# Kernel optimization log

Measured on AMD Instinct MI355X. Metric: run time of the kernel, lower is better.

Reference implementation:

```python
import jax, jax.numpy as jnp
import numpy as np
from jax import lax

N, L, V, ES, HS = 16384, 512, 32000, 32, 64


def setup_inputs() -> dict:
    key = jax.random.key(0)
    k_tok, k_len, k_emb, k_wih, k_whh, k_bih, k_bhh = jax.random.split(key, 7)
    # valid tokens in [1, V) so that (x != 0).sum(1) == true prefix length
    tok = jax.random.randint(k_tok, (N, L), 1, V)
    lengths = jax.random.randint(k_len, (N,), 0, L + 1)  # includes empty seqs
    x = jnp.where(jnp.arange(L)[None, :] < lengths[:, None], tok, 0)
    s = 0.1
    embedding = jax.random.normal(k_emb, (V, ES), dtype=jnp.float32) * s
    w_ih = jax.random.normal(k_wih, (3 * HS, ES), dtype=jnp.float32) * s  # [r|z|n] stacked (torch order)
    w_hh = jax.random.normal(k_whh, (3 * HS, HS), dtype=jnp.float32) * s
    b_ih = jax.random.normal(k_bih, (3 * HS,), dtype=jnp.float32) * s
    b_hh = jax.random.normal(k_bhh, (3 * HS,), dtype=jnp.float32) * s
    return {"x": x, "embedding": embedding, "w_ih": w_ih, "w_hh": w_hh,
            "b_ih": b_ih, "b_hh": b_hh}


def reference(x, embedding, w_ih, w_hh, b_ih, b_hh):
    # Faithful math: final GRU hidden state over the nonzero prefix of each row;
    # rows with length 0 return zeros (h0). Equivalent to bucketed
    # pack_padded_sequence + GRU + scatter of final hidden states.
    n, l = x.shape
    hs = w_hh.shape[1]
    lengths = (x != 0).sum(axis=1)  # [n]

    def step(h, inp):
        t, xt = inp                      # xt: [n] token ids at time t
        e = embedding[xt]                # [n, es] gather
        gx = e @ w_ih.T + b_ih           # [n, 3*hs]
        gh = h @ w_hh.T + b_hh           # [n, 3*hs]
        xr, xz, xn = jnp.split(gx, 3, axis=-1)
        hr, hz, hn = jnp.split(gh, 3, axis=-1)
        r = jax.nn.sigmoid(xr + hr)
        z = jax.nn.sigmoid(xz + hz)
        ng = jnp.tanh(xn + r * hn)
        h_new = (1.0 - z) * ng + z * h   # torch GRU update
        h = jnp.where((t < lengths)[:, None], h_new, h)  # freeze past length
        return h, None

    h0 = jnp.zeros((n, hs), dtype=embedding.dtype)
    hT, _ = lax.scan(step, h0, (jnp.arange(l), x.T))
    return hT
```

## Files before the change

kernel.cpp:

```cpp
#include <hip/hip_runtime.h>

#define N_SEQ 16384
#define LSEQ  512
#define VOCAB 32000
#define ES    32
#define HS    64
#define LDH   72

#define SC_RZ (-1.4426950408889634f)
#define SC_N  (-2.8853900817779268f)

typedef _Float16 v8h __attribute__((ext_vector_type(8)));
typedef float    v4f __attribute__((ext_vector_type(4)));

#define NLB (N_SEQ / 4)
#define NEB (VOCAB * ES / 256)
__global__ __launch_bounds__(256) void k_prep(const int* __restrict__ x,
                                              const float* __restrict__ emb,
                                              const float* __restrict__ whh,
                                              const float* __restrict__ wih,
                                              int* __restrict__ len,
                                              int* __restrict__ hist,
                                              _Float16* __restrict__ ef,
                                              _Float16* __restrict__ wpk,
                                              _Float16* __restrict__ wpe){
  int b = blockIdx.x;
  if (b < NLB){
    int wid  = (b * 256 + threadIdx.x) >> 6;
    int lane = threadIdx.x & 63;
    const int* xr = x + (size_t)wid * LSEQ;
    int cnt = 0;
    #pragma unroll
    for (int j = 0; j < 8; ++j) cnt += (xr[lane + 64*j] != 0) ? 1 : 0;
    #pragma unroll
    for (int o = 32; o; o >>= 1) cnt += __shfl_down(cnt, o, 64);
    if (lane == 0){ len[wid] = cnt; atomicAdd(&hist[cnt], 1); }
  } else if (b < NLB + NEB){
    int i = (b - NLB) * 256 + threadIdx.x;
    ef[i] = (_Float16)emb[i];
  } else if (b < NLB + NEB + 6){
    int tid = (b - NLB - NEB) * 256 + threadIdx.x;
    int f = tid >> 6, l = tid & 63;
    int jt = f >> 1, kf = f & 1;
    float sc = (jt < 8) ? SC_RZ : SC_N;
    #pragma unroll
    for (int i = 0; i < 8; ++i){
      int row = jt * 16 + (l & 15);
      int col = kf * 32 + (l >> 4) * 8 + i;
      wpk[(size_t)tid * 8 + i] = (_Float16)(sc * whh[row * HS + col]);
    }
  } else {
    int tid = (b - NLB - NEB - 6) * 256 + threadIdx.x;
    int tile = tid >> 6, l = tid & 63;
    float sc = ((tile >> 2) < 2) ? SC_RZ : SC_N;
    #pragma unroll
    for (int i = 0; i < 8; ++i){
      int row = tile * 16 + (l & 15);
      int col = (l >> 4) * 8 + i;
      wpe[(size_t)tid * 8 + i] = (_Float16)(sc * wih[row * ES + col]);
    }
  }
}

__global__ __launch_bounds__(1024) void k_sort(const int* __restrict__ hist,
                                               const int* __restrict__ len,
                                               int* __restrict__ perm){
  __shared__ int buf[1024];
  __shared__ int offs[513];
  int i = threadIdx.x;
  buf[i] = (i < 513) ? hist[i] : 0;
  __syncthreads();
  for (int d = 1; d < 1024; d <<= 1){
    int v = (i >= d) ? buf[i - d] : 0;
    __syncthreads();
    buf[i] += v;
    __syncthreads();
  }
  if (i < 513) offs[i] = (i == 0) ? 0 : buf[i - 1];
  __syncthreads();
  for (int s = i; s < N_SEQ; s += 1024){
    int l = len[s];
    int pos = atomicAdd(&offs[l], 1);
    perm[pos] = s;
  }
}

__global__ __launch_bounds__(256, 4) void k_gru(
    const int* __restrict__ x, const _Float16* __restrict__ ef,
    const _Float16* __restrict__ wpk, const _Float16* __restrict__ wpe,
    const float* __restrict__ bih, const float* __restrict__ bhh,
    const int* __restrict__ perm, const int* __restrict__ len,
    float* __restrict__ out)
{
  __shared__ __align__(16) _Float16 hb[2][16 * LDH];
  int qt   = threadIdx.x >> 6;
  int w = blockIdx.x >> 8, cq = blockIdx.x & 255;
  int rank = w * 256 + ((w & 1) ? (255 - cq) : cq);
  int grp  = 1023 - rank;
  int lane = threadIdx.x & 63;
  int q = lane >> 4, c = lane & 15;
  int uu = qt*16 + c;

  v8h bfh[3][2], bfe[3];
  #pragma unroll
  for (int g = 0; g < 3; ++g){
    int tile = g*4 + qt;
    #pragma unroll
    for (int kf = 0; kf < 2; ++kf)
      bfh[g][kf] = *(const v8h*)(wpk + ((size_t)(tile*2 + kf)*64 + lane)*8);
    bfe[g] = *(const v8h*)(wpe + ((size_t)tile*64 + lane)*8);
  }

  int sq[4], ln[4];
  #pragma unroll
  for (int r = 0; r < 4; ++r){
    int s = perm[grp * 16 + q*4 + r];
    sq[r] = s;
    ln[r] = len[s];
  }
  float br  = SC_RZ * (bih[uu]      + bhh[uu]);
  float bz  = SC_RZ * (bih[HS + uu] + bhh[HS + uu]);
  float ben = SC_N  *  bih[2*HS + uu];
  float bhn = SC_N  *  bhh[2*HS + uu];
  v4f brq  = {br, br, br, br};
  v4f bzq  = {bz, bz, bz, bz};
  v4f benq = {ben, ben, ben, ben};
  v4f bhnq = {bhn, bhn, bhn, bhn};

  float h[4];
  #pragma unroll
  for (int r = 0; r < 4; ++r) h[r] = 0.f;

  for (int i = threadIdx.x; i < 16*LDH; i += 256) hb[0][i] = (_Float16)0.f;
  __syncthreads();

  int tmax = max(max(ln[0], ln[1]), max(ln[2], ln[3]));
  tmax = max(tmax, __shfl_xor(tmax, 16, 64));
  tmax = max(tmax, __shfl_xor(tmax, 32, 64));
  int tmin = min(min(ln[0], ln[1]), min(ln[2], ln[3]));
  tmin = min(tmin, __shfl_xor(tmin, 16, 64));
  tmin = min(tmin, __shfl_xor(tmin, 32, 64));

  const int* xr = x + (size_t)perm[grp * 16 + c] * LSEQ;

  v8h aec, aen;
  int tk1, tk2;
  v4f pra, prb, pza, pzb, dea, deb;
  {
    int tk0 = xr[0];
    aec = *(const v8h*)(ef + (size_t)tk0 * ES + q*8);
    tk1 = xr[1];
    pra = __builtin_amdgcn_mfma_f32_16x16x32_f16(aec, bfe[0], brq,  0,0,0);
    pza = __builtin_amdgcn_mfma_f32_16x16x32_f16(aec, bfe[1], bzq,  0,0,0);
    dea = __builtin_amdgcn_mfma_f32_16x16x32_f16(aec, bfe[2], benq, 0,0,0);
  }

  #define LDS_BARRIER() __asm__ volatile("s_waitcnt lgkmcnt(0)\n\ts_barrier" ::: "memory")

  #define GRU_STEP(FREEZE, AEN, PRR, PRZ, DEN, PRRn, PRZn, DENn, TKN_, TKNN_, RB, WB) \
  {                                                                            \
    AEN = *(const v8h*)(ef + (size_t)TKN_ * ES + q*8);       \
    int t2 = min(t + 2, LSEQ - 1);                                             \
    TKNN_ = xr[t2];                                             \
    v8h a0 = *(const v8h*)(&hb[RB][c*LDH + q*8]);                              \
    v8h a1 = *(const v8h*)(&hb[RB][c*LDH + 32 + q*8]);                         \
    v4f zr  = __builtin_amdgcn_mfma_f32_16x16x32_f16(a1, bfh[0][1], PRR, 0,0,0);\
    v4f Dr  = __builtin_amdgcn_mfma_f32_16x16x32_f16(a0, bfh[0][0], zr,  0,0,0);\
    v4f zz  = __builtin_amdgcn_mfma_f32_16x16x32_f16(a1, bfh[1][1], PRZ, 0,0,0);\
    v4f Dz  = __builtin_amdgcn_mfma_f32_16x16x32_f16(a0, bfh[1][0], zz,  0,0,0);\
    v4f zh  = __builtin_amdgcn_mfma_f32_16x16x32_f16(a1, bfh[2][1], bhnq,0,0,0);\
    v4f Dhn = __builtin_amdgcn_mfma_f32_16x16x32_f16(a0, bfh[2][0], zh,  0,0,0);\
    _Pragma("unroll")                                                          \
    for (int r = 0; r < 4; ++r){                                               \
      float rg   = __builtin_amdgcn_rcpf(1.f + __builtin_amdgcn_exp2f(Dr[r])); \
      float zg   = __builtin_amdgcn_rcpf(1.f + __builtin_amdgcn_exp2f(Dz[r])); \
      float te   = __builtin_amdgcn_exp2f(DEN[r] + rg * Dhn[r]);               \
      float ng   = fmaf(2.f, __builtin_amdgcn_rcpf(1.f + te), -1.f);           \
      float hnew = ng + zg * (h[r] - ng);                                      \
      h[r]       = (FREEZE && t >= ln[r]) ? h[r] : hnew;                       \
    }                                                                          \
    PRRn = __builtin_amdgcn_mfma_f32_16x16x32_f16(AEN, bfe[0], brq,  0,0,0);   \
    PRZn = __builtin_amdgcn_mfma_f32_16x16x32_f16(AEN, bfe[1], bzq,  0,0,0);   \
    DENn = __builtin_amdgcn_mfma_f32_16x16x32_f16(AEN, bfe[2], benq, 0,0,0);   \
    _Pragma("unroll")                                                          \
    for (int r = 0; r < 4; ++r)                                                \
      hb[WB][(q*4 + r)*LDH + uu] = (_Float16)h[r];                             \
    LDS_BARRIER();                                                             \
  }

  int t = 0;
  for (; t + 1 < tmin; ){
    GRU_STEP(0, aen, pra, pza, dea, prb, pzb, deb, tk1, tk2, 0, 1); ++t;
    GRU_STEP(0, aec, prb, pzb, deb, pra, pza, dea, tk2, tk1, 1, 0); ++t;
  }
  for (; t + 1 < tmax; ){
    GRU_STEP(1, aen, pra, pza, dea, prb, pzb, deb, tk1, tk2, 0, 1); ++t;
    GRU_STEP(1, aec, prb, pzb, deb, pra, pza, dea, tk2, tk1, 1, 0); ++t;
  }
  if (t < tmax){
    GRU_STEP(1, aen, pra, pza, dea, prb, pzb, deb, tk1, tk2, 0, 1); ++t;
  }
  #undef GRU_STEP
  #undef LDS_BARRIER

  #pragma unroll
  for (int r = 0; r < 4; ++r)
    out[(size_t)sq[r] * HS + uu] = h[r];
}

extern "C" void kernel_launch(void* const* d_in, const int* in_sizes, int n_in,
                              void* d_out, int out_size, void* d_ws, size_t ws_size,
                              hipStream_t stream){
  const int*   x   = (const int*)  d_in[0];
  const float* emb = (const float*)d_in[1];
  const float* wih = (const float*)d_in[2];
  const float* whh = (const float*)d_in[3];
  const float* bih = (const float*)d_in[4];
  const float* bhh = (const float*)d_in[5];
  float* out = (float*)d_out;

  char* ws = (char*)d_ws;
  size_t off = 0;
  _Float16* ef  = (_Float16*)(ws + off);  off += (size_t)VOCAB * ES * sizeof(_Float16);
  _Float16* wpk = (_Float16*)(ws + off);  off += (size_t)24 * 64 * 8 * sizeof(_Float16);
  _Float16* wpe = (_Float16*)(ws + off);  off += (size_t)12 * 64 * 8 * sizeof(_Float16);
  off = (off + 255) & ~(size_t)255;
  int* len  = (int*)(ws + off);           off += (size_t)N_SEQ * sizeof(int);
  int* perm = (int*)(ws + off);           off += (size_t)N_SEQ * sizeof(int);
  int* hist = (int*)(ws + off);           off += 513 * sizeof(int);

  hipMemsetAsync(hist, 0, 513 * sizeof(int), stream);
  k_prep <<<NLB + NEB + 9, 256, 0, stream>>>(x, emb, whh, wih, len, hist, ef, wpk, wpe);
  k_sort <<<1,            1024, 0, stream>>>(hist, len, perm);
  k_gru  <<<N_SEQ / 16,    256, 0, stream>>>(x, ef, wpk, wpe, bih, bhh, perm, len, out);
}
```

Baseline: 331.9 us.

## Binary-search lengths, parallel scatter sort, and stage tokens in LDS

Sequence lengths are now found with a per-thread binary search over each row, relying on the prefix-of-nonzeros structure, instead of a full 512-element wave scan. The single-block counting sort becomes a 16-block scatter that uses global atomic counters. The GRU kernel preloads all 16×512 tokens of its group into shared memory as 16-bit values, so each step reads its token from LDS rather than global memory, and the asm barrier becomes __syncthreads. This removes a large part of the prep traffic and the per-step global token latency. It costs 16KB of extra LDS per block, which may lower occupancy, plus an upfront token load in every block.

```diff
diff --git a/kernel.cpp b/kernel.cpp
--- a/kernel.cpp
+++ b/kernel.cpp
@@ -13,7 +13,7 @@
 typedef _Float16 v8h __attribute__((ext_vector_type(8)));
 typedef float    v4f __attribute__((ext_vector_type(4)));
 
-#define NLB (N_SEQ / 4)
+#define NLB (N_SEQ / 256)
 #define NEB (VOCAB * ES / 256)
 __global__ __launch_bounds__(256) void k_prep(const int* __restrict__ x,
                                               const float* __restrict__ emb,
@@ -26,15 +26,12 @@
                                               _Float16* __restrict__ wpe){
   int b = blockIdx.x;
   if (b < NLB){
-    int wid  = (b * 256 + threadIdx.x) >> 6;
-    int lane = threadIdx.x & 63;
-    const int* xr = x + (size_t)wid * LSEQ;
-    int cnt = 0;
-    #pragma unroll
-    for (int j = 0; j < 8; ++j) cnt += (xr[lane + 64*j] != 0) ? 1 : 0;
-    #pragma unroll
-    for (int o = 32; o; o >>= 1) cnt += __shfl_down(cnt, o, 64);
-    if (lane == 0){ len[wid] = cnt; atomicAdd(&hist[cnt], 1); }
+    int row = b * 256 + threadIdx.x;
+    const int* xr = x + (size_t)row * LSEQ;
+    int lo = 0, hi = LSEQ;
+    while (lo < hi){ int mid = (lo + hi) >> 1; if (xr[mid] != 0) lo = mid + 1; else hi = mid; }
+    len[row] = lo;
+    atomicAdd(&hist[lo], 1);
   } else if (b < NLB + NEB){
     int i = (b - NLB) * 256 + threadIdx.x;
     ef[i] = (_Float16)emb[i];
@@ -62,9 +59,10 @@
   }
 }
 
-__global__ __launch_bounds__(1024) void k_sort(const int* __restrict__ hist,
-                                               const int* __restrict__ len,
-                                               int* __restrict__ perm){
+__global__ __launch_bounds__(1024) void k_scatter(const int* __restrict__ hist,
+                                                  const int* __restrict__ len,
+                                                  int* __restrict__ gcnt,
+                                                  int* __restrict__ perm){
   __shared__ int buf[1024];
   __shared__ int offs[513];
   int i = threadIdx.x;
@@ -78,11 +76,10 @@
   }
   if (i < 513) offs[i] = (i == 0) ? 0 : buf[i - 1];
   __syncthreads();
-  for (int s = i; s < N_SEQ; s += 1024){
-    int l = len[s];
-    int pos = atomicAdd(&offs[l], 1);
-    perm[pos] = s;
-  }
+  int s = blockIdx.x * 1024 + i;
+  int l = len[s];
+  int pos = offs[l] + atomicAdd(&gcnt[l], 1);
+  perm[pos] = s;
 }
 
 __global__ __launch_bounds__(256, 4) void k_gru(
@@ -93,6 +90,7 @@
     float* __restrict__ out)
 {
   __shared__ __align__(16) _Float16 hb[2][16 * LDH];
+  __shared__ unsigned short tok[16 * LSEQ];
   int qt   = threadIdx.x >> 6;
   int w = blockIdx.x >> 8, cq = blockIdx.x & 255;
   int rank = w * 256 + ((w & 1) ? (255 - cq) : cq);
@@ -132,6 +130,11 @@
   for (int r = 0; r < 4; ++r) h[r] = 0.f;
 
   for (int i = threadIdx.x; i < 16*LDH; i += 256) hb[0][i] = (_Float16)0.f;
+
+  for (int j = threadIdx.x; j < 16*LSEQ; j += 256){
+    int s = j >> 9, tt = j & (LSEQ-1);
+    tok[j] = (unsigned short)x[(size_t)perm[grp*16 + s] * LSEQ + tt];
+  }
   __syncthreads();
 
   int tmax = max(max(ln[0], ln[1]), max(ln[2], ln[3]));
@@ -141,27 +144,23 @@
   tmin = min(tmin, __shfl_xor(tmin, 16, 64));
   tmin = min(tmin, __shfl_xor(tmin, 32, 64));
 
-  const int* xr = x + (size_t)perm[grp * 16 + c] * LSEQ;
+  const unsigned short* tkr = tok + c * LSEQ;
 
   v8h aec, aen;
-  int tk1, tk2;
   v4f pra, prb, pza, pzb, dea, deb;
   {
-    int tk0 = xr[0];
+    int tk0 = tkr[0];
     aec = *(const v8h*)(ef + (size_t)tk0 * ES + q*8);
-    tk1 = xr[1];
     pra = __builtin_amdgcn_mfma_f32_16x16x32_f16(aec, bfe[0], brq,  0,0,0);
     pza = __builtin_amdgcn_mfma_f32_16x16x32_f16(aec, bfe[1], bzq,  0,0,0);
     dea = __builtin_amdgcn_mfma_f32_16x16x32_f16(aec, bfe[2], benq, 0,0,0);
-  }
-
-  #define LDS_BARRIER() __asm__ volatile("s_waitcnt lgkmcnt(0)\n\ts_barrier" ::: "memory")
-
-  #define GRU_STEP(FREEZE, AEN, PRR, PRZ, DEN, PRRn, PRZn, DENn, TKN_, TKNN_, RB, WB) \
+    int tk1 = tkr[1];
+    aen = *(const v8h*)(ef + (size_t)tk1 * ES + q*8);
+  }
+
+  #define GRU_STEP(FREEZE, ACONS, ALOAD, PRR, PRZ, DEN, PRRn, PRZn, DENn, RB, WB) \
   {                                                                            \
-    AEN = *(const v8h*)(ef + (size_t)TKN_ * ES + q*8);       \
-    int t2 = min(t + 2, LSEQ - 1);                                             \
-    TKNN_ = xr[t2];                                             \
+    int tkn = tkr[(t + 2) & (LSEQ-1)];                                         \
     v8h a0 = *(const v8h*)(&hb[RB][c*LDH + q*8]);                              \
     v8h a1 = *(const v8h*)(&hb[RB][c*LDH + 32 + q*8]);                         \
     v4f zr  = __builtin_amdgcn_mfma_f32_16x16x32_f16(a1, bfh[0][1], PRR, 0,0,0);\
@@ -179,29 +178,29 @@
       float hnew = ng + zg * (h[r] - ng);                                      \
       h[r]       = (FREEZE && t >= ln[r]) ? h[r] : hnew;                       \
     }                                                                          \
-    PRRn = __builtin_amdgcn_mfma_f32_16x16x32_f16(AEN, bfe[0], brq,  0,0,0);   \
-    PRZn = __builtin_amdgcn_mfma_f32_16x16x32_f16(AEN, bfe[1], bzq,  0,0,0);   \
-    DENn = __builtin_amdgcn_mfma_f32_16x16x32_f16(AEN, bfe[2], benq, 0,0,0);   \
+    PRRn = __builtin_amdgcn_mfma_f32_16x16x32_f16(ACONS, bfe[0], brq,  0,0,0); \
+    PRZn = __builtin_amdgcn_mfma_f32_16x16x32_f16(ACONS, bfe[1], bzq,  0,0,0); \
+    DENn = __builtin_amdgcn_mfma_f32_16x16x32_f16(ACONS, bfe[2], benq, 0,0,0); \
+    ALOAD = *(const v8h*)(ef + (size_t)tkn * ES + q*8);           \
     _Pragma("unroll")                                                          \
     for (int r = 0; r < 4; ++r)                                                \
       hb[WB][(q*4 + r)*LDH + uu] = (_Float16)h[r];                             \
-    LDS_BARRIER();                                                             \
+    __syncthreads();                                                           \
   }
 
   int t = 0;
   for (; t + 1 < tmin; ){
-    GRU_STEP(0, aen, pra, pza, dea, prb, pzb, deb, tk1, tk2, 0, 1); ++t;
-    GRU_STEP(0, aec, prb, pzb, deb, pra, pza, dea, tk2, tk1, 1, 0); ++t;
+    GRU_STEP(0, aen, aec, pra, pza, dea, prb, pzb, deb, 0, 1); ++t;
+    GRU_STEP(0, aec, aen, prb, pzb, deb, pra, pza, dea, 1, 0); ++t;
   }
   for (; t + 1 < tmax; ){
-    GRU_STEP(1, aen, pra, pza, dea, prb, pzb, deb, tk1, tk2, 0, 1); ++t;
-    GRU_STEP(1, aec, prb, pzb, deb, pra, pza, dea, tk2, tk1, 1, 0); ++t;
+    GRU_STEP(1, aen, aec, pra, pza, dea, prb, pzb, deb, 0, 1); ++t;
+    GRU_STEP(1, aec, aen, prb, pzb, deb, pra, pza, dea, 1, 0); ++t;
   }
   if (t < tmax){
-    GRU_STEP(1, aen, pra, pza, dea, prb, pzb, deb, tk1, tk2, 0, 1); ++t;
+    GRU_STEP(1, aen, aec, pra, pza, dea, prb, pzb, deb, 0, 1); ++t;
   }
   #undef GRU_STEP
-  #undef LDS_BARRIER
 
   #pragma unroll
   for (int r = 0; r < 4; ++r)
@@ -228,9 +227,10 @@
   int* len  = (int*)(ws + off);           off += (size_t)N_SEQ * sizeof(int);
   int* perm = (int*)(ws + off);           off += (size_t)N_SEQ * sizeof(int);
   int* hist = (int*)(ws + off);           off += 513 * sizeof(int);
-
-  hipMemsetAsync(hist, 0, 513 * sizeof(int), stream);
-  k_prep <<<NLB + NEB + 9, 256, 0, stream>>>(x, emb, whh, wih, len, hist, ef, wpk, wpe);
-  k_sort <<<1,            1024, 0, stream>>>(hist, len, perm);
-  k_gru  <<<N_SEQ / 16,    256, 0, stream>>>(x, ef, wpk, wpe, bih, bhh, perm, len, out);
-}
+  int* gcnt = (int*)(ws + off);           off += 513 * sizeof(int);
+
+  hipMemsetAsync(hist, 0, 2 * 513 * sizeof(int), stream);
+  k_prep   <<<NLB + NEB + 9, 256, 0, stream>>>(x, emb, whh, wih, len, hist, ef, wpk, wpe);
+  k_scatter<<<N_SEQ / 1024, 1024, 0, stream>>>(hist, len, gcnt, perm);
+  k_gru    <<<N_SEQ / 16,    256, 0, stream>>>(x, ef, wpk, wpe, bih, bhh, perm, len, out);
+}
```

Result: faster. 310.3 us (-6.5%).
